# Performance work log

Hardware: AMD Instinct MI355X
Metric: run time of the kernel (lower is better)

## Reference

```python
import jax, jax.numpy as jnp
import numpy as np

N, D, NUM_CLASSES = 4096, 1024, 100
CHUNK = 16  # rows per block; block intermediate is CHUNK x N x D (~256 MB fp32)


def setup_inputs() -> dict:
    key = jax.random.key(0)
    k1, k2 = jax.random.split(key)
    feats = jax.random.uniform(k1, (N, D), dtype=jnp.float32)
    labels = jax.random.randint(k2, (N,), 0, NUM_CLASSES)
    image_idxs = jnp.arange(N)
    return {"feats": feats, "labels": labels, "image_idxs": image_idxs,
            "normalize_feats": 1}


def _cheb_dist(feats):
    """All-pairs Chebyshev distance, computed in row blocks to avoid an N x N x D tensor."""
    n, d = feats.shape
    chunks = feats.reshape(n // CHUNK, CHUNK, d)

    def row_block(fc):  # fc: [CHUNK, D] -> [CHUNK, N]
        return jnp.max(jnp.abs(fc[:, None, :] - feats[None, :, :]), axis=2)

    return jax.lax.map(row_block, chunks).reshape(n, n)  # dist[i, j] = max_d |f_i - f_j|


def reference(feats, labels, image_idxs, normalize_feats):
    n = feats.shape[0]
    feats = feats.reshape(n, -1)
    if normalize_feats:
        feats = feats / jnp.max(feats, axis=1, keepdims=True)
    dist = _cheb_dist(feats)                      # symmetric [N, N]
    same_label = labels[:, None] == labels[None, :]
    masked = jnp.where(same_label, jnp.inf, dist)  # mask same-label rows per column
    closest_idx = jnp.argmin(masked, axis=0)       # hardest different-label negative per column
    loss = dist[jnp.arange(n), closest_idx].mean()
    closest_pairs = image_idxs[closest_idx]
    return loss, closest_pairs
```

## Files before the change

### kernel.cpp

```cpp
#include <hip/hip_runtime.h>
#include <hip/hip_bf16.h>
#include <cfloat>

#define NROWS 4096
#define DDIM 1024
#define NT 64
#define NBLK (NT * (NT + 1) / 2)
#define NSLOT (NT + 1)

#define MAX3ABS(ACC, X, Y) \
    asm("v_max3_f32 %0, abs(%1), abs(%2), %0" : "+v"(ACC) : "v"(X), "v"(Y))

#define MERGE(BV, BI, V, I) \
    do { if ((V) < (BV) || ((V) == (BV) && (I) < (BI))) { BV = (V); BI = (I); } } while (0)

__global__ __launch_bounds__(256) void normalize_kernel(const float* __restrict__ feats,
                                                        const int* __restrict__ normflag,
                                                        float* __restrict__ normf) {
    const int wave = threadIdx.x >> 6;
    const int lane = threadIdx.x & 63;
    const int row  = blockIdx.x * 4 + wave;
    const float* fr = feats + (size_t)row * DDIM;
    float*       fw = normf + (size_t)row * DDIM;
    float4 v[4];
    float m = 0.0f;
#pragma unroll
    for (int k = 0; k < 4; ++k) {
        v[k] = *(const float4*)(fr + lane * 4 + k * 256);
        m = fmaxf(fmaxf(fmaxf(m, v[k].x), fmaxf(v[k].y, v[k].z)), v[k].w);
    }
#pragma unroll
    for (int off = 32; off > 0; off >>= 1) m = fmaxf(m, __shfl_xor(m, off));
    const float r = (*normflag != 0) ? m : 1.0f;
#pragma unroll
    for (int k = 0; k < 4; ++k) {
        v[k].x /= r; v[k].y /= r; v[k].z /= r; v[k].w /= r;
        *(float4*)(fw + lane * 4 + k * 256) = v[k];
    }
}

__global__ __launch_bounds__(256) void rowmax_kernel(const float* __restrict__ feats,
                                                     const int* __restrict__ normflag,
                                                     float* __restrict__ rowmax) {
    const int wave = threadIdx.x >> 6;
    const int lane = threadIdx.x & 63;
    const int row  = blockIdx.x * 4 + wave;
    const float* fr = feats + (size_t)row * DDIM;
    float m = 0.0f;
    for (int d = lane * 4; d < DDIM; d += 256) {
        float4 v = *(const float4*)(fr + d);
        m = fmaxf(fmaxf(fmaxf(m, v.x), fmaxf(v.y, v.z)), v.w);
    }
#pragma unroll
    for (int off = 32; off > 0; off >>= 1) m = fmaxf(m, __shfl_xor(m, off));
    if (lane == 0) rowmax[row] = (*normflag != 0) ? m : 1.0f;
}

template <bool NORM>
__global__ __launch_bounds__(256, 5) void cheb_kernel(const float* __restrict__ src,
                                                      const float* __restrict__ rowmax,
                                                      const int* __restrict__ labels,
                                                      float* __restrict__ pval,
                                                      int* __restrict__ pidx) {
    int bid = blockIdx.x;
    bid = (bid & 7) * (NBLK / 8) + (bid >> 3);
    float fs = sqrtf((float)((2 * NT + 1) * (2 * NT + 1) - 8 * bid));
    int ta = (int)(((float)(2 * NT + 1) - fs) * 0.5f);
    while ((ta + 1) * NT - ((ta + 1) * ta) / 2 <= bid) ++ta;
    while (ta * NT - (ta * (ta - 1)) / 2 > bid) --ta;
    const int tb = ta + (bid - (ta * NT - (ta * (ta - 1)) / 2));
    const int iBase = ta * 64;
    const int jBase = tb * 64;

    const int t   = threadIdx.x;
    const int w   = t >> 6;
    const int rH  = (w & 1) * 32;
    const int cH  = (w >> 1) * 32;
    const int ty8 = t & 7;
    const int tx8 = (t >> 3) & 7;

    __shared__ __align__(16) float As[64 * 32];
    __shared__ __align__(16) float Bs[64 * 32];
    __shared__ float sval[4 * 32];
    __shared__ int   sidx[4 * 32];

    int lA[4], lB[4];
#pragma unroll
    for (int kk = 0; kk < 4; ++kk) lA[kk] = labels[iBase + rH + ty8 + 8 * kk];
#pragma unroll
    for (int jj = 0; jj < 4; ++jj) lB[jj] = labels[jBase + cH + tx8 + 8 * jj];

    float acc[4][4];
#pragma unroll
    for (int kk = 0; kk < 4; ++kk)
#pragma unroll
        for (int jj = 0; jj < 4; ++jj) acc[kk][jj] = 0.0f;

    const int r0  = t >> 3;
    const int q0  = t & 7;
    const int lo0 = r0 * 32 + 4 * (q0 ^ (r0 & 7));
    const int lo1 = (r0 + 32) * 32 + 4 * (q0 ^ ((r0 + 32) & 7));
    const float* gA0 = src + (size_t)(iBase + r0) * DDIM + 4 * q0;
    const float* gA1 = src + (size_t)(iBase + r0 + 32) * DDIM + 4 * q0;
    const float* gB0 = src + (size_t)(jBase + r0) * DDIM + 4 * q0;
    const float* gB1 = src + (size_t)(jBase + r0 + 32) * DDIM + 4 * q0;
    float rA0 = 1.0f, rA1 = 1.0f, rB0 = 1.0f, rB1 = 1.0f;
    if (NORM) {
        rA0 = rowmax[iBase + r0]; rA1 = rowmax[iBase + r0 + 32];
        rB0 = rowmax[jBase + r0]; rB1 = rowmax[jBase + r0 + 32];
    }

    for (int dc = 0; dc < DDIM / 32; ++dc) {
        const int dB = dc * 32;
        __syncthreads();
        {
            float4 va0 = *(const float4*)(gA0 + dB);
            float4 va1 = *(const float4*)(gA1 + dB);
            float4 vb0 = *(const float4*)(gB0 + dB);
            float4 vb1 = *(const float4*)(gB1 + dB);
            if (NORM) {
                va0.x /= rA0; va0.y /= rA0; va0.z /= rA0; va0.w /= rA0;
                va1.x /= rA1; va1.y /= rA1; va1.z /= rA1; va1.w /= rA1;
                vb0.x /= rB0; vb0.y /= rB0; vb0.z /= rB0; vb0.w /= rB0;
                vb1.x /= rB1; vb1.y /= rB1; vb1.z /= rB1; vb1.w /= rB1;
            }
            *(float4*)(As + lo0) = va0;
            *(float4*)(As + lo1) = va1;
            *(float4*)(Bs + lo0) = vb0;
            *(float4*)(Bs + lo1) = vb1;
        }
        __syncthreads();

#pragma unroll
        for (int q = 0; q < 8; ++q) {
            float4 a[4], b[4];
#pragma unroll
            for (int kk = 0; kk < 4; ++kk)
                a[kk] = *(const float4*)(As + (rH + ty8 + 8 * kk) * 32 + 4 * (q ^ ty8));
#pragma unroll
            for (int jj = 0; jj < 4; ++jj)
                b[jj] = *(const float4*)(Bs + (cH + tx8 + 8 * jj) * 32 + 4 * (q ^ tx8));
#pragma unroll
            for (int kk = 0; kk < 4; ++kk)
#pragma unroll
                for (int jj = 0; jj < 4; ++jj) {
                    const float d0 = a[kk].x - b[jj].x;
                    const float d1 = a[kk].y - b[jj].y;
                    const float d2 = a[kk].z - b[jj].z;
                    const float d3 = a[kk].w - b[jj].w;
                    MAX3ABS(acc[kk][jj], d0, d1);
                    MAX3ABS(acc[kk][jj], d2, d3);
                }
        }
    }

    {
        float bv1[4]; int bi1[4];
#pragma unroll
        for (int jj = 0; jj < 4; ++jj) {
            float bv = FLT_MAX; int bi = 0x7fffffff;
#pragma unroll
            for (int kk = 0; kk < 4; ++kk) {
                const int i = iBase + rH + ty8 + 8 * kk;
                const float v = (lA[kk] == lB[jj]) ? FLT_MAX : acc[kk][jj];
                MERGE(bv, bi, v, i);
            }
#pragma unroll
            for (int off = 1; off <= 4; off <<= 1) {
                const float ov = __shfl_xor(bv, off);
                const int   oi = __shfl_xor(bi, off);
                MERGE(bv, bi, ov, oi);
            }
            bv1[jj] = bv; bi1[jj] = bi;
        }
        if (ty8 == 0) {
#pragma unroll
            for (int jj = 0; jj < 4; ++jj) {
                const int cq = tx8 + 8 * jj;
                sval[w * 32 + cq] = bv1[jj];
                sidx[w * 32 + cq] = bi1[jj];
            }
        }
    }
    __syncthreads();
    if (t < 64) {
        const int C = t, ch = C >> 5, cq = C & 31;
        const int w1 = ch * 2, w2 = ch * 2 + 1;
        float bv = sval[w1 * 32 + cq]; int bi = sidx[w1 * 32 + cq];
        MERGE(bv, bi, sval[w2 * 32 + cq], sidx[w2 * 32 + cq]);
        pval[ta * NROWS + jBase + C] = bv;
        pidx[ta * NROWS + jBase + C] = bi;
    }
    __syncthreads();

#pragma unroll
    for (int kk = 0; kk < 4; ++kk) {
        float bv = FLT_MAX; int bi = 0x7fffffff;
#pragma unroll
        for (int jj = 0; jj < 4; ++jj) {
            const int j = jBase + cH + tx8 + 8 * jj;
            const float v = (lA[kk] == lB[jj]) ? FLT_MAX : acc[kk][jj];
            MERGE(bv, bi, v, j);
        }
#pragma unroll
        for (int off = 8; off <= 32; off <<= 1) {
            const float ov = __shfl_xor(bv, off);
            const int   oi = __shfl_xor(bi, off);
            MERGE(bv, bi, ov, oi);
        }
        if (((t >> 3) & 7) == 0) {
            const int rq = ty8 + 8 * kk;
            sval[w * 32 + rq] = bv;
            sidx[w * 32 + rq] = bi;
        }
    }
    __syncthreads();
    if (t < 64) {
        const int R = t, rh = R >> 5, rq = R & 31;
        const int w1 = rh, w2 = rh + 2;
        float bv = sval[w1 * 32 + rq]; int bi = sidx[w1 * 32 + rq];
        MERGE(bv, bi, sval[w2 * 32 + rq], sidx[w2 * 32 + rq]);
        pval[(tb + 1) * NROWS + iBase + R] = bv;
        pidx[(tb + 1) * NROWS + iBase + R] = bi;
    }
}

__global__ __launch_bounds__(256) void finalizeA_kernel(const float* __restrict__ pval,
                                                        const int* __restrict__ pidx,
                                                        const int* __restrict__ image_idxs,
                                                        float* __restrict__ out,
                                                        float* __restrict__ colmin) {
    const int j = blockIdx.x * 256 + threadIdx.x;
    float bv = FLT_MAX; int bi = 0x7fffffff;
    for (int s = 0; s < NSLOT; ++s) {
        const float v = pval[s * NROWS + j];
        const int   i = pidx[s * NROWS + j];
        MERGE(bv, bi, v, i);
    }
    out[1 + j] = (float)image_idxs[bi];
    colmin[j] = bv;
}

__global__ __launch_bounds__(256) void finalizeB_kernel(const float* __restrict__ colmin,
                                                        float* __restrict__ out) {
    const int t = threadIdx.x;
    float s = 0.0f;
#pragma unroll
    for (int k = 0; k < 16; ++k) s += colmin[t + 256 * k];
#pragma unroll
    for (int off = 32; off > 0; off >>= 1) s += __shfl_xor(s, off);
    __shared__ float ss[4];
    if ((t & 63) == 0) ss[t >> 6] = s;
    __syncthreads();
    if (t == 0) out[0] = (ss[0] + ss[1] + ss[2] + ss[3]) / (float)NROWS;
}

extern "C" void kernel_launch(void* const* d_in, const int* in_sizes, int n_in,
                              void* d_out, int out_size, void* d_ws, size_t ws_size,
                              hipStream_t stream) {
    const float* feats      = (const float*)d_in[0];
    const int*   labels     = (const int*)d_in[1];
    const int*   image_idxs = (const int*)d_in[2];
    const int*   normflag   = (const int*)d_in[3];
    float*       out        = (float*)d_out;

    const size_t normBytes = (size_t)NROWS * DDIM * sizeof(float);
    const size_t partBytes = (size_t)NSLOT * NROWS * 8 + NROWS * 4;

    if (ws_size >= normBytes + partBytes) {
        float* normf  = (float*)d_ws;
        float* pval   = (float*)((char*)d_ws + normBytes);
        int*   pidx   = (int*)(pval + NSLOT * NROWS);
        float* colmin = (float*)(pidx + NSLOT * NROWS);
        normalize_kernel<<<NROWS / 4, 256, 0, stream>>>(feats, normflag, normf);
        cheb_kernel<false><<<NBLK, 256, 0, stream>>>(normf, nullptr, labels, pval, pidx);
        finalizeA_kernel<<<NROWS / 256, 256, 0, stream>>>(pval, pidx, image_idxs, out, colmin);
        finalizeB_kernel<<<1, 256, 0, stream>>>(colmin, out);
    } else {
        float* rowmax = (float*)d_ws;
        float* pval   = rowmax + NROWS;
        int*   pidx   = (int*)(pval + NSLOT * NROWS);
        float* colmin = (float*)(pidx + NSLOT * NROWS);
        rowmax_kernel<<<NROWS / 4, 256, 0, stream>>>(feats, normflag, rowmax);
        cheb_kernel<true><<<NBLK, 256, 0, stream>>>(feats, rowmax, labels, pval, pidx);
        finalizeA_kernel<<<NROWS / 256, 256, 0, stream>>>(pval, pidx, image_idxs, out, colmin);
        finalizeB_kernel<<<1, 256, 0, stream>>>(colmin, out);
    }
}
```

Baseline: 328.9 us.

## Use single-wave 64x64 tiles with 8x8 per-thread register blocking

The Chebyshev tile kernel moves from 256 threads with 4x4 accumulators per thread to one 64-lane wave per 64x64 tile, each lane holding an 8x8 accumulator block. This doubles the reuse of each shared-memory float4 load and removes the cross-wave shared-memory reduction and its barriers in the argmin epilogue, since shuffles within one wave now suffice. The cost is far more registers per thread (64 accumulators plus 8 B vectors), fewer threads per tile to hide LDS and global load latency, and a serialized global-to-LDS fill done by a single wave.

Result: slower. 438.3 us (+33.3%).

```diff
diff --git a/kernel.cpp b/kernel.cpp
--- a/kernel.cpp
+++ b/kernel.cpp
@@ -57,11 +57,11 @@
 }
 
 template <bool NORM>
-__global__ __launch_bounds__(256, 5) void cheb_kernel(const float* __restrict__ src,
-                                                      const float* __restrict__ rowmax,
-                                                      const int* __restrict__ labels,
-                                                      float* __restrict__ pval,
-                                                      int* __restrict__ pidx) {
+__global__ __launch_bounds__(64, 3) void cheb_kernel(const float* __restrict__ src,
+                                                     const float* __restrict__ rowmax,
+                                                     const int* __restrict__ labels,
+                                                     float* __restrict__ pval,
+                                                     int* __restrict__ pidx) {
     int bid = blockIdx.x;
     bid = (bid & 7) * (NBLK / 8) + (bid >> 3);
     float fs = sqrtf((float)((2 * NT + 1) * (2 * NT + 1) - 8 * bid));
@@ -72,133 +72,111 @@
     const int iBase = ta * 64;
     const int jBase = tb * 64;
 
-    const int t   = threadIdx.x;
-    const int w   = t >> 6;
-    const int rH  = (w & 1) * 32;
-    const int cH  = (w >> 1) * 32;
-    const int ty8 = t & 7;
-    const int tx8 = (t >> 3) & 7;
+    const int lane = threadIdx.x;
+    const int ty8  = lane & 7;
+    const int tx8  = lane >> 3;
 
     __shared__ __align__(16) float As[64 * 32];
     __shared__ __align__(16) float Bs[64 * 32];
-    __shared__ float sval[4 * 32];
-    __shared__ int   sidx[4 * 32];
-
-    int lA[4], lB[4];
-#pragma unroll
-    for (int kk = 0; kk < 4; ++kk) lA[kk] = labels[iBase + rH + ty8 + 8 * kk];
-#pragma unroll
-    for (int jj = 0; jj < 4; ++jj) lB[jj] = labels[jBase + cH + tx8 + 8 * jj];
-
-    float acc[4][4];
-#pragma unroll
-    for (int kk = 0; kk < 4; ++kk)
-#pragma unroll
-        for (int jj = 0; jj < 4; ++jj) acc[kk][jj] = 0.0f;
-
-    const int r0  = t >> 3;
-    const int q0  = t & 7;
-    const int lo0 = r0 * 32 + 4 * (q0 ^ (r0 & 7));
-    const int lo1 = (r0 + 32) * 32 + 4 * (q0 ^ ((r0 + 32) & 7));
-    const float* gA0 = src + (size_t)(iBase + r0) * DDIM + 4 * q0;
-    const float* gA1 = src + (size_t)(iBase + r0 + 32) * DDIM + 4 * q0;
-    const float* gB0 = src + (size_t)(jBase + r0) * DDIM + 4 * q0;
-    const float* gB1 = src + (size_t)(jBase + r0 + 32) * DDIM + 4 * q0;
-    float rA0 = 1.0f, rA1 = 1.0f, rB0 = 1.0f, rB1 = 1.0f;
+
+    float acc[8][8];
+#pragma unroll
+    for (int kk = 0; kk < 8; ++kk)
+#pragma unroll
+        for (int jj = 0; jj < 8; ++jj) acc[kk][jj] = 0.0f;
+
+    const int r0 = lane >> 3;
+    const int q0 = lane & 7;
+    float* Aw = As + r0 * 32 + 4 * (q0 ^ r0);
+    float* Bw = Bs + r0 * 32 + 4 * (q0 ^ r0);
+    const float* gA = src + (size_t)(iBase + r0) * DDIM + 4 * q0;
+    const float* gB = src + (size_t)(jBase + r0) * DDIM + 4 * q0;
+    float rmA[8], rmB[8];
     if (NORM) {
-        rA0 = rowmax[iBase + r0]; rA1 = rowmax[iBase + r0 + 32];
-        rB0 = rowmax[jBase + r0]; rB1 = rowmax[jBase + r0 + 32];
-    }
+#pragma unroll
+        for (int p = 0; p < 8; ++p) {
+            rmA[p] = rowmax[iBase + r0 + 8 * p];
+            rmB[p] = rowmax[jBase + r0 + 8 * p];
+        }
+    }
+
+    const char* Ab = (const char*)As + ty8 * 128;
+    const char* Bb = (const char*)Bs + tx8 * 128;
 
     for (int dc = 0; dc < DDIM / 32; ++dc) {
         const int dB = dc * 32;
         __syncthreads();
-        {
-            float4 va0 = *(const float4*)(gA0 + dB);
-            float4 va1 = *(const float4*)(gA1 + dB);
-            float4 vb0 = *(const float4*)(gB0 + dB);
-            float4 vb1 = *(const float4*)(gB1 + dB);
+#pragma unroll 2
+        for (int p = 0; p < 8; ++p) {
+            float4 va = *(const float4*)(gA + (size_t)p * 8 * DDIM + dB);
+            float4 vb = *(const float4*)(gB + (size_t)p * 8 * DDIM + dB);
             if (NORM) {
-                va0.x /= rA0; va0.y /= rA0; va0.z /= rA0; va0.w /= rA0;
-                va1.x /= rA1; va1.y /= rA1; va1.z /= rA1; va1.w /= rA1;
-                vb0.x /= rB0; vb0.y /= rB0; vb0.z /= rB0; vb0.w /= rB0;
-                vb1.x /= rB1; vb1.y /= rB1; vb1.z /= rB1; vb1.w /= rB1;
+                va.x /= rmA[p]; va.y /= rmA[p]; va.z /= rmA[p]; va.w /= rmA[p];
+                vb.x /= rmB[p]; vb.y /= rmB[p]; vb.z /= rmB[p]; vb.w /= rmB[p];
             }
-            *(float4*)(As + lo0) = va0;
-            *(float4*)(As + lo1) = va1;
-            *(float4*)(Bs + lo0) = vb0;
-            *(float4*)(Bs + lo1) = vb1;
+            *(float4*)(Aw + p * 256) = va;
+            *(float4*)(Bw + p * 256) = vb;
         }
         __syncthreads();
 
-#pragma unroll
+#pragma unroll 2
         for (int q = 0; q < 8; ++q) {
-            float4 a[4], b[4];
-#pragma unroll
-            for (int kk = 0; kk < 4; ++kk)
-                a[kk] = *(const float4*)(As + (rH + ty8 + 8 * kk) * 32 + 4 * (q ^ ty8));
-#pragma unroll
-            for (int jj = 0; jj < 4; ++jj)
-                b[jj] = *(const float4*)(Bs + (cH + tx8 + 8 * jj) * 32 + 4 * (q ^ tx8));
-#pragma unroll
-            for (int kk = 0; kk < 4; ++kk)
-#pragma unroll
-                for (int jj = 0; jj < 4; ++jj) {
-                    const float d0 = a[kk].x - b[jj].x;
-                    const float d1 = a[kk].y - b[jj].y;
-                    const float d2 = a[kk].z - b[jj].z;
-                    const float d3 = a[kk].w - b[jj].w;
+            const int oa = 16 * (q ^ ty8);
+            const int ob = 16 * (q ^ tx8);
+            float4 b[8];
+#pragma unroll
+            for (int jj = 0; jj < 8; ++jj)
+                b[jj] = *(const float4*)(Bb + jj * 1024 + ob);
+#pragma unroll
+            for (int kk = 0; kk < 8; ++kk) {
+                const float4 a = *(const float4*)(Ab + kk * 1024 + oa);
+#pragma unroll
+                for (int jj = 0; jj < 8; ++jj) {
+                    const float d0 = a.x - b[jj].x;
+                    const float d1 = a.y - b[jj].y;
+                    const float d2 = a.z - b[jj].z;
+                    const float d3 = a.w - b[jj].w;
                     MAX3ABS(acc[kk][jj], d0, d1);
                     MAX3ABS(acc[kk][jj], d2, d3);
                 }
-        }
-    }
-
-    {
-        float bv1[4]; int bi1[4];
-#pragma unroll
-        for (int jj = 0; jj < 4; ++jj) {
-            float bv = FLT_MAX; int bi = 0x7fffffff;
-#pragma unroll
-            for (int kk = 0; kk < 4; ++kk) {
-                const int i = iBase + rH + ty8 + 8 * kk;
-                const float v = (lA[kk] == lB[jj]) ? FLT_MAX : acc[kk][jj];
-                MERGE(bv, bi, v, i);
             }
-#pragma unroll
-            for (int off = 1; off <= 4; off <<= 1) {
-                const float ov = __shfl_xor(bv, off);
-                const int   oi = __shfl_xor(bi, off);
-                MERGE(bv, bi, ov, oi);
-            }
-            bv1[jj] = bv; bi1[jj] = bi;
+        }
+    }
+
+    int lA[8], lB[8];
+#pragma unroll
+    for (int kk = 0; kk < 8; ++kk) lA[kk] = labels[iBase + ty8 + 8 * kk];
+#pragma unroll
+    for (int jj = 0; jj < 8; ++jj) lB[jj] = labels[jBase + tx8 + 8 * jj];
+
+#pragma unroll
+    for (int jj = 0; jj < 8; ++jj) {
+        float bv = FLT_MAX; int bi = 0x7fffffff;
+#pragma unroll
+        for (int kk = 0; kk < 8; ++kk) {
+            const int i = iBase + ty8 + 8 * kk;
+            const float v = (lA[kk] == lB[jj]) ? FLT_MAX : acc[kk][jj];
+            MERGE(bv, bi, v, i);
+        }
+#pragma unroll
+        for (int off = 1; off <= 4; off <<= 1) {
+            const float ov = __shfl_xor(bv, off);
+            const int   oi = __shfl_xor(bi, off);
+            MERGE(bv, bi, ov, oi);
         }
         if (ty8 == 0) {
-#pragma unroll
-            for (int jj = 0; jj < 4; ++jj) {
-                const int cq = tx8 + 8 * jj;
-                sval[w * 32 + cq] = bv1[jj];
-                sidx[w * 32 + cq] = bi1[jj];
-            }
-        }
-    }
-    __syncthreads();
-    if (t < 64) {
-        const int C = t, ch = C >> 5, cq = C & 31;
-        const int w1 = ch * 2, w2 = ch * 2 + 1;
-        float bv = sval[w1 * 32 + cq]; int bi = sidx[w1 * 32 + cq];
-        MERGE(bv, bi, sval[w2 * 32 + cq], sidx[w2 * 32 + cq]);
-        pval[ta * NROWS + jBase + C] = bv;
-        pidx[ta * NROWS + jBase + C] = bi;
-    }
-    __syncthreads();
-
-#pragma unroll
-    for (int kk = 0; kk < 4; ++kk) {
+            const int j = jBase + tx8 + 8 * jj;
+            pval[ta * NROWS + j] = bv;
+            pidx[ta * NROWS + j] = bi;
+        }
+    }
+
+#pragma unroll
+    for (int kk = 0; kk < 8; ++kk) {
         float bv = FLT_MAX; int bi = 0x7fffffff;
 #pragma unroll
-        for (int jj = 0; jj < 4; ++jj) {
-            const int j = jBase + cH + tx8 + 8 * jj;
+        for (int jj = 0; jj < 8; ++jj) {
+            const int j = jBase + tx8 + 8 * jj;
             const float v = (lA[kk] == lB[jj]) ? FLT_MAX : acc[kk][jj];
             MERGE(bv, bi, v, j);
         }
@@ -208,20 +186,11 @@
             const int   oi = __shfl_xor(bi, off);
             MERGE(bv, bi, ov, oi);
         }
-        if (((t >> 3) & 7) == 0) {
-            const int rq = ty8 + 8 * kk;
-            sval[w * 32 + rq] = bv;
-            sidx[w * 32 + rq] = bi;
-        }
-    }
-    __syncthreads();
-    if (t < 64) {
-        const int R = t, rh = R >> 5, rq = R & 31;
-        const int w1 = rh, w2 = rh + 2;
-        float bv = sval[w1 * 32 + rq]; int bi = sidx[w1 * 32 + rq];
-        MERGE(bv, bi, sval[w2 * 32 + rq], sidx[w2 * 32 + rq]);
-        pval[(tb + 1) * NROWS + iBase + R] = bv;
-        pidx[(tb + 1) * NROWS + iBase + R] = bi;
+        if (tx8 == 0) {
+            const int i = iBase + ty8 + 8 * kk;
+            pval[(tb + 1) * NROWS + i] = bv;
+            pidx[(tb + 1) * NROWS + i] = bi;
+        }
     }
 }
 
@@ -273,7 +242,7 @@
         int*   pidx   = (int*)(pval + NSLOT * NROWS);
         float* colmin = (float*)(pidx + NSLOT * NROWS);
         normalize_kernel<<<NROWS / 4, 256, 0, stream>>>(feats, normflag, normf);
-        cheb_kernel<false><<<NBLK, 256, 0, stream>>>(normf, nullptr, labels, pval, pidx);
+        cheb_kernel<false><<<NBLK, 64, 0, stream>>>(normf, nullptr, labels, pval, pidx);
         finalizeA_kernel<<<NROWS / 256, 256, 0, stream>>>(pval, pidx, image_idxs, out, colmin);
         finalizeB_kernel<<<1, 256, 0, stream>>>(colmin, out);
     } else {
@@ -282,7 +251,7 @@
         int*   pidx   = (int*)(pval + NSLOT * NROWS);
         float* colmin = (float*)(pidx + NSLOT * NROWS);
         rowmax_kernel<<<NROWS / 4, 256, 0, stream>>>(feats, normflag, rowmax);
-        cheb_kernel<true><<<NBLK, 256, 0, stream>>>(feats, rowmax, labels, pval, pidx);
+        cheb_kernel<true><<<NBLK, 64, 0, stream>>>(feats, rowmax, labels, pval, pidx);
         finalizeA_kernel<<<NROWS / 256, 256, 0, stream>>>(pval, pidx, image_idxs, out, colmin);
         finalizeB_kernel<<<1, 256, 0, stream>>>(colmin, out);
     }
```
